# Kernel optimization log

Hardware: AMD Instinct MI355X
Metric: run time of the kernel (lower is better)

## Reference

```python
import math
import jax, jax.numpy as jnp
import numpy as np
from jax import lax

FS = 16000.0
TAU_FAST_MS = 2.0
TAU_SLOW_MS = 60.0
EPS = 1e-6


def setup_inputs() -> dict:
    key = jax.random.key(0)
    B, C, T = 8, 64, 64000
    x = jax.random.normal(key, (B, C, T), dtype=jnp.float32)
    mu_fast = jnp.float32(1.0 - math.exp(-1.0 / (FS * TAU_FAST_MS / 1000.0)))
    mu_slow = jnp.float32(1.0 - math.exp(-1.0 / (FS * TAU_SLOW_MS / 1000.0)))
    mix_weight_adapt = jnp.float32(0.5)
    mix_weight_hp = jnp.float32(0.3)
    return {
        "x": x,
        "mu_fast": mu_fast,
        "mu_slow": mu_slow,
        "mix_weight_adapt": mix_weight_adapt,
        "mix_weight_hp": mix_weight_hp,
    }


def reference(x, mu_fast, mu_slow, mix_weight_adapt, mix_weight_hp):
    # x: [B, C, T]
    x = jnp.maximum(x, 0.0)
    xt = jnp.moveaxis(x, -1, 0)  # [T, B, C], time-leading for scan

    def step(carry, xcur):
        mf, ms = carry
        mf = (1.0 - mu_fast) * mf + mu_fast * xcur
        ms = (1.0 - mu_slow) * ms + mu_slow * xcur
        return (mf, ms), (mf, ms)

    init = (xt[0], xt[0])  # EMA initialized at first sample
    _, (mf_rest, ms_rest) = lax.scan(step, init, xt[1:])
    M_fast = jnp.concatenate([xt[:1], mf_rest], axis=0)  # [T, B, C]
    M_slow = jnp.concatenate([xt[:1], ms_rest], axis=0)

    mix_adapt = jax.nn.sigmoid(mix_weight_adapt)
    M = mix_adapt * M_fast + (1.0 - mix_adapt) * M_slow
    M = jnp.moveaxis(M, 0, -1)  # back to [B, C, T]

    x_adapted = x / (EPS + M)
    x_hp = x - M
    mix_hp = jax.nn.sigmoid(mix_weight_hp)
    return x_adapted + mix_hp * x_hp
```

## Files before the change

kernel.cpp:

```cpp
#include <hip/hip_runtime.h>


#define THREADS 256
#define WPB 4
#define K 25
#define WTILE (64 * K)
#define T_LEN 64000
#define SEGS_W 8
#define SEG_LEN (T_LEN / SEGS_W)
#define SEG_TILES (SEG_LEN / WTILE)
#define HALO_TILES 4
#define EPS_V 1e-6f

typedef float nfloat4 __attribute__((ext_vector_type(4)));

__device__ __forceinline__ float rfl(float v) {
    return __int_as_float(__builtin_amdgcn_readfirstlane(__float_as_int(v)));
}

__global__ __launch_bounds__(THREADS, 4)
void dual_ema_hp_kernel(const float* __restrict__ x,
                        const float* __restrict__ p_mu_fast,
                        const float* __restrict__ p_mu_slow,
                        const float* __restrict__ p_mwa,
                        const float* __restrict__ p_mhp,
                        float* __restrict__ out)
{
    __shared__ float lds[WPB * WTILE];
    const int tid  = threadIdx.x;
    const int lane = tid & 63;
    const int wv   = tid >> 6;
    float* buf = &lds[wv * WTILE];

    const int gw  = blockIdx.x * WPB + wv;
    const int row = gw / SEGS_W;
    const int seg = gw % SEGS_W;
    const int h   = (seg == 0) ? 0 : HALO_TILES;
    const int nt  = SEG_TILES + h;

    const float* gseg = x   + (size_t)row * T_LEN + (size_t)seg * SEG_LEN - (size_t)h * WTILE;
    float*       oseg = out + (size_t)row * T_LEN + (size_t)seg * SEG_LEN - (size_t)h * WTILE;

    const float mu_f = rfl(p_mu_fast[0]);
    const float mu_s = rfl(p_mu_slow[0]);
    const float af = rfl(1.0f - mu_f);
    const float as = rfl(1.0f - mu_s);
    const float wa  = rfl(1.0f / (1.0f + __expf(-p_mwa[0])));
    const float wb  = rfl(1.0f - wa);
    const float whp = rfl(1.0f / (1.0f + __expf(-p_mhp[0])));

    const float Pf1  = rfl(__powf(af, (float)K));
    const float Ps1  = rfl(__powf(as, (float)K));
    const float Pf2  = rfl(Pf1 * Pf1),   Ps2  = rfl(Ps1 * Ps1);
    const float Pf4  = rfl(Pf2 * Pf2),   Ps4  = rfl(Ps2 * Ps2);
    const float Pf8  = rfl(Pf4 * Pf4),   Ps8  = rfl(Ps4 * Ps4);
    const float Pf16 = rfl(Pf8 * Pf8),   Ps16 = rfl(Ps8 * Ps8);
    const float Pf32 = rfl(Pf16 * Pf16), Ps32 = rfl(Ps16 * Ps16);

    float4 p0, p1, p2, p3, p4, p5; float ps;
    {
        const float4* g4 = (const float4*)gseg;
        p0 = g4[0 * 64 + lane]; p1 = g4[1 * 64 + lane]; p2 = g4[2 * 64 + lane];
        p3 = g4[3 * 64 + lane]; p4 = g4[4 * 64 + lane]; p5 = g4[5 * 64 + lane];
        ps = gseg[1536 + lane];
    }
    {
        float4* i4 = (float4*)buf;
        i4[0 * 64 + lane] = p0; i4[1 * 64 + lane] = p1; i4[2 * 64 + lane] = p2;
        i4[3 * 64 + lane] = p3; i4[4 * 64 + lane] = p4; i4[5 * 64 + lane] = p5;
        buf[1536 + lane] = ps;
    }

    float sfr = 0.0f, ssr = 0.0f;

    for (int t = 0; t < nt; ++t) {
        asm volatile("s_waitcnt lgkmcnt(0)" ::: "memory");

        if (seg == 0 && t == 0 && lane == 0) {
            float y0 = fmaxf(buf[0], 0.0f);
            sfr = y0; ssr = y0;
        }

        const bool pref = (t + 1 < nt);
        if (pref) {
            const float* gt = gseg + (size_t)(t + 1) * WTILE;
            const float4* g4 = (const float4*)gt;
            p0 = g4[0 * 64 + lane]; p1 = g4[1 * 64 + lane]; p2 = g4[2 * 64 + lane];
            p3 = g4[3 * 64 + lane]; p4 = g4[4 * 64 + lane]; p5 = g4[5 * 64 + lane];
            ps = gt[1536 + lane];
        }

        float inf = (lane == 0) ? sfr : 0.0f;
        float ins = (lane == 0) ? ssr : 0.0f;
        float mf, ms;
        {
            float yv = fmaxf(buf[lane * K], 0.0f);
            mf = fmaf(af, inf, mu_f * yv);
            ms = fmaf(as, ins, mu_s * yv);
        }
#pragma unroll
        for (int i = 1; i < K; ++i) {
            float yv = fmaxf(buf[lane * K + i], 0.0f);
            mf = fmaf(af, mf, mu_f * yv);
            ms = fmaf(as, ms, mu_s * yv);
        }

        float cf = mf, cs = ms, uf, us;
        uf = __shfl_up(cf, 1);  us = __shfl_up(cs, 1);
        cf = (lane >= 1)  ? fmaf(Pf1,  uf, cf) : cf;  cs = (lane >= 1)  ? fmaf(Ps1,  us, cs) : cs;
        uf = __shfl_up(cf, 2);  us = __shfl_up(cs, 2);
        cf = (lane >= 2)  ? fmaf(Pf2,  uf, cf) : cf;  cs = (lane >= 2)  ? fmaf(Ps2,  us, cs) : cs;
        uf = __shfl_up(cf, 4);  us = __shfl_up(cs, 4);
        cf = (lane >= 4)  ? fmaf(Pf4,  uf, cf) : cf;  cs = (lane >= 4)  ? fmaf(Ps4,  us, cs) : cs;
        uf = __shfl_up(cf, 8);  us = __shfl_up(cs, 8);
        cf = (lane >= 8)  ? fmaf(Pf8,  uf, cf) : cf;  cs = (lane >= 8)  ? fmaf(Ps8,  us, cs) : cs;
        uf = __shfl_up(cf, 16); us = __shfl_up(cs, 16);
        cf = (lane >= 16) ? fmaf(Pf16, uf, cf) : cf;  cs = (lane >= 16) ? fmaf(Ps16, us, cs) : cs;
        uf = __shfl_up(cf, 32); us = __shfl_up(cs, 32);
        cf = (lane >= 32) ? fmaf(Pf32, uf, cf) : cf;  cs = (lane >= 32) ? fmaf(Ps32, us, cs) : cs;

        float ex_f = __shfl_up(cf, 1), ex_s = __shfl_up(cs, 1);
        if (lane == 0) { ex_f = sfr; ex_s = ssr; }
        sfr = __shfl(cf, 63);
        ssr = __shfl(cs, 63);

        asm volatile("s_waitcnt lgkmcnt(0)" ::: "memory");

        const bool emit = (t >= h);
        if (emit) {
            float mf2 = ex_f, ms2 = ex_s;
#pragma unroll
            for (int i = 0; i < K; ++i) {
                float yv = fmaxf(buf[lane * K + i], 0.0f);
                mf2 = fmaf(af, mf2, mu_f * yv);
                ms2 = fmaf(as, ms2, mu_s * yv);
                float M = fmaf(wa, mf2, wb * ms2);
                float o = yv * __builtin_amdgcn_rcpf(EPS_V + M) + whp * (yv - M);
                buf[lane * K + i] = o;
            }
            asm volatile("s_waitcnt lgkmcnt(0)" ::: "memory");

            float* gout = oseg + (size_t)t * WTILE;
            nfloat4* go4 = (nfloat4*)gout;
            const nfloat4* o4 = (const nfloat4*)buf;
#pragma unroll
            for (int c = 0; c < 6; ++c) {
                nfloat4 v = o4[c * 64 + lane];
                __builtin_nontemporal_store(v, &go4[c * 64 + lane]);
            }
            __builtin_nontemporal_store(buf[1536 + lane], &gout[1536 + lane]);
        }

        if (pref) {
            float4* i4 = (float4*)buf;
            i4[0 * 64 + lane] = p0; i4[1 * 64 + lane] = p1; i4[2 * 64 + lane] = p2;
            i4[3 * 64 + lane] = p3; i4[4 * 64 + lane] = p4; i4[5 * 64 + lane] = p5;
            buf[1536 + lane] = ps;
        }
    }
}

extern "C" void kernel_launch(void* const* d_in, const int* in_sizes, int n_in,
                              void* d_out, int out_size, void* d_ws, size_t ws_size,
                              hipStream_t stream) {
    const float* x    = (const float*)d_in[0];
    const float* mu_f = (const float*)d_in[1];
    const float* mu_s = (const float*)d_in[2];
    const float* mwa  = (const float*)d_in[3];
    const float* mhp  = (const float*)d_in[4];
    float* out = (float*)d_out;

    const int rows   = in_sizes[0] / T_LEN;
    const int blocks = rows * SEGS_W / WPB;
    dual_ema_hp_kernel<<<blocks, THREADS, 0, stream>>>(x, mu_f, mu_s, mwa, mhp, out);
}
```

Baseline: 251.4 us.

## Stage input tiles with global_load_lds into double-buffered LDS

Replaces the register-staged prefetch (global float4 loads then LDS writes) with direct global-to-LDS dword loads into two ping-pong LDS buffers per wave, using vmcnt waits to sync. The goal is to drop the extra VGPR round-trip and the LDS write instructions, and to overlap the next tile's load with compute. Block size drops to 128 threads (2 waves) because each wave now needs twice the LDS. The risks are dword-granular loads (25 per tile instead of 7) and fragile vmcnt counting, since the nontemporal output stores also count against vmcnt.

```diff
diff --git a/kernel.cpp b/kernel.cpp
--- a/kernel.cpp
+++ b/kernel.cpp
@@ -1,8 +1,8 @@
 #include <hip/hip_runtime.h>
 
 
-#define THREADS 256
-#define WPB 4
+#define THREADS 128
+#define WPB 2
 #define K 25
 #define WTILE (64 * K)
 #define T_LEN 64000
@@ -18,7 +18,20 @@
     return __int_as_float(__builtin_amdgcn_readfirstlane(__float_as_int(v)));
 }
 
-__global__ __launch_bounds__(THREADS, 4)
+__device__ __forceinline__ void gll_dword(const float* g, float* l) {
+    __builtin_amdgcn_global_load_lds(
+        (const __attribute__((address_space(1))) unsigned int*)g,
+        (__attribute__((address_space(3))) unsigned int*)l,
+        4, 0, 0);
+}
+
+__device__ __forceinline__ void stage(const float* gt, float* b, int lane) {
+#pragma unroll
+    for (int c = 0; c < K; ++c)
+        gll_dword(gt + c * 64 + lane, b + c * 64);
+}
+
+__global__ __launch_bounds__(THREADS, 2)
 void dual_ema_hp_kernel(const float* __restrict__ x,
                         const float* __restrict__ p_mu_fast,
                         const float* __restrict__ p_mu_slow,
@@ -26,11 +39,12 @@
                         const float* __restrict__ p_mhp,
                         float* __restrict__ out)
 {
-    __shared__ float lds[WPB * WTILE];
+    __shared__ __align__(16) float lds[WPB * 2 * WTILE];
     const int tid  = threadIdx.x;
     const int lane = tid & 63;
     const int wv   = tid >> 6;
-    float* buf = &lds[wv * WTILE];
+    float* buf0 = &lds[wv * 2 * WTILE];
+    float* buf1 = buf0 + WTILE;
 
     const int gw  = blockIdx.x * WPB + wv;
     const int row = gw / SEGS_W;
@@ -57,38 +71,25 @@
     const float Pf16 = rfl(Pf8 * Pf8),   Ps16 = rfl(Ps8 * Ps8);
     const float Pf32 = rfl(Pf16 * Pf16), Ps32 = rfl(Ps16 * Ps16);
 
-    float4 p0, p1, p2, p3, p4, p5; float ps;
-    {
-        const float4* g4 = (const float4*)gseg;
-        p0 = g4[0 * 64 + lane]; p1 = g4[1 * 64 + lane]; p2 = g4[2 * 64 + lane];
-        p3 = g4[3 * 64 + lane]; p4 = g4[4 * 64 + lane]; p5 = g4[5 * 64 + lane];
-        ps = gseg[1536 + lane];
-    }
-    {
-        float4* i4 = (float4*)buf;
-        i4[0 * 64 + lane] = p0; i4[1 * 64 + lane] = p1; i4[2 * 64 + lane] = p2;
-        i4[3 * 64 + lane] = p3; i4[4 * 64 + lane] = p4; i4[5 * 64 + lane] = p5;
-        buf[1536 + lane] = ps;
-    }
+    stage(gseg, buf0, lane);
+    stage(gseg + WTILE, buf1, lane);
+    asm volatile("s_waitcnt vmcnt(25)" ::: "memory");
 
     float sfr = 0.0f, ssr = 0.0f;
 
     for (int t = 0; t < nt; ++t) {
-        asm volatile("s_waitcnt lgkmcnt(0)" ::: "memory");
+        float* buf = (t & 1) ? buf1 : buf0;
+
+        if (t > h)       { asm volatile("s_waitcnt vmcnt(7)" ::: "memory"); }
+        else if (t > 0)  { asm volatile("s_waitcnt vmcnt(0)" ::: "memory"); }
 
         if (seg == 0 && t == 0 && lane == 0) {
             float y0 = fmaxf(buf[0], 0.0f);
             sfr = y0; ssr = y0;
         }
 
-        const bool pref = (t + 1 < nt);
-        if (pref) {
-            const float* gt = gseg + (size_t)(t + 1) * WTILE;
-            const float4* g4 = (const float4*)gt;
-            p0 = g4[0 * 64 + lane]; p1 = g4[1 * 64 + lane]; p2 = g4[2 * 64 + lane];
-            p3 = g4[3 * 64 + lane]; p4 = g4[4 * 64 + lane]; p5 = g4[5 * 64 + lane];
-            ps = gt[1536 + lane];
-        }
+        if (t >= 1 && t + 1 < nt)
+            stage(gseg + (size_t)(t + 1) * WTILE, (t & 1) ? buf0 : buf1, lane);
 
         float inf = (lane == 0) ? sfr : 0.0f;
         float ins = (lane == 0) ? ssr : 0.0f;
@@ -150,13 +151,6 @@
             }
             __builtin_nontemporal_store(buf[1536 + lane], &gout[1536 + lane]);
         }
-
-        if (pref) {
-            float4* i4 = (float4*)buf;
-            i4[0 * 64 + lane] = p0; i4[1 * 64 + lane] = p1; i4[2 * 64 + lane] = p2;
-            i4[3 * 64 + lane] = p3; i4[4 * 64 + lane] = p4; i4[5 * 64 + lane] = p5;
-            buf[1536 + lane] = ps;
-        }
     }
 }
 
```

After: 258.4 us. 1.03x slower.
